# Optimization experiments

Hardware: AMD Instinct MI355X
Metric: run time of the kernel (lower is better)

Reference implementation:

```python
import jax, jax.numpy as jnp
import numpy as np

N_NODES = 40000
N_EDGES = 640000
BATCH = 2
IN_DIM = 3
HID = 128
OUT_DIM = 3


def setup_inputs() -> dict:
    key = jax.random.key(0)
    ks = jax.random.split(key, 16)
    p = jax.random.normal(ks[0], (BATCH, N_NODES, IN_DIM), dtype=jnp.float32)
    edge_rows = jax.random.randint(ks[1], (N_EDGES,), 0, N_NODES, dtype=jnp.int32)
    edge_cols = jax.random.randint(ks[2], (N_EDGES,), 0, N_NODES, dtype=jnp.int32)
    # normalize_sparse_matrix: divide each nonzero (value 1.0) by the row's nonzero count
    deg = jax.ops.segment_sum(jnp.ones((N_EDGES,), jnp.float32), edge_rows, num_segments=N_NODES)
    adj_vals = 1.0 / deg[edge_rows]  # every used row has deg >= 1
    s = 0.05
    # initial Linear(3 -> 128)
    W_init = jax.random.normal(ks[3], (IN_DIM, HID), jnp.float32) * s
    b_init = jnp.zeros((HID,), jnp.float32)
    # 4 GraphConvs inside the two blocks (all 128->128), each has filter + self_filter
    Wf_blocks = jax.random.normal(ks[4], (4, HID, HID), jnp.float32) * s
    bf_blocks = jnp.zeros((4, HID), jnp.float32)
    Ws_blocks = jax.random.normal(ks[5], (4, HID, HID), jnp.float32) * s
    bs_blocks = jnp.zeros((4, HID), jnp.float32)
    # final GraphConvLayer (128 -> 3)
    Wf_out = jax.random.normal(ks[6], (HID, OUT_DIM), jnp.float32) * s
    bf_out = jnp.zeros((OUT_DIM,), jnp.float32)
    Ws_out = jax.random.normal(ks[7], (HID, OUT_DIM), jnp.float32) * s
    bs_out = jnp.zeros((OUT_DIM,), jnp.float32)
    return dict(p=p, adj_vals=adj_vals, edge_rows=edge_rows, edge_cols=edge_cols,
                W_init=W_init, b_init=b_init,
                Wf_blocks=Wf_blocks, bf_blocks=bf_blocks,
                Ws_blocks=Ws_blocks, bs_blocks=bs_blocks,
                Wf_out=Wf_out, bf_out=bf_out, Ws_out=Ws_out, bs_out=bs_out)


def reference(p, adj_vals, edge_rows, edge_cols,
              W_init, b_init,
              Wf_blocks, bf_blocks, Ws_blocks, bs_blocks,
              Wf_out, bf_out, Ws_out, bs_out):
    n = p.shape[1]

    def spmm(xb):  # xb: [N, d] -> A @ xb via edge-list scatter-add
        return jax.ops.segment_sum(adj_vals[:, None] * xb[edge_cols], edge_rows, num_segments=n)

    spmm_b = jax.vmap(spmm)  # [B, N, d]

    def gconv(x, Wf, bf, Ws, bs):
        # sparse path: self_filter(x) + filter(spmm(adj, x))
        return (x @ Ws + bs) + (spmm_b(x) @ Wf + bf)

    x = p @ W_init + b_init  # [B, N, HID]
    for blk in range(2):  # two GraphConvBlocks, residual, no shortcut (dims equal)
        net = gconv(jax.nn.relu(x), Wf_blocks[2 * blk], bf_blocks[2 * blk],
                    Ws_blocks[2 * blk], bs_blocks[2 * blk])
        dx = gconv(jax.nn.relu(net), Wf_blocks[2 * blk + 1], bf_blocks[2 * blk + 1],
                   Ws_blocks[2 * blk + 1], bs_blocks[2 * blk + 1])
        x = x + dx
    # final GraphConvLayer 128 -> 3
    out = gconv(jax.nn.relu(x), Wf_out, bf_out, Ws_out, bs_out)
    return out
```

## Files before the change

### kernel.cpp

```cpp
#include <hip/hip_runtime.h>


typedef unsigned short u16;
typedef unsigned int   u32;
typedef __bf16 bf8_t __attribute__((ext_vector_type(8)));
typedef float  f4_t  __attribute__((ext_vector_type(4)));

#define N_NODES 40000
#define N_EDGES 640000
#define BN      80000

__device__ __forceinline__ float bf2f(u16 u) {
  union { u32 i; float f; } v; v.i = ((u32)u) << 16; return v.f;
}
__device__ __forceinline__ u16 f2bf(float f) {
  union { float f; u32 i; } v; v.f = f;
  u32 i = v.i;
  return (u16)((i + 0x7FFFu + ((i >> 16) & 1u)) >> 16);
}
__device__ __forceinline__ float asf(u32 i) {
  union { u32 u; float f; } v; v.u = i; return v.f;
}
__device__ __forceinline__ u32 pack2(float a, float b) {
  return (u32)f2bf(a) | ((u32)f2bf(b) << 16);
}

__global__ void fill_kernel(float* __restrict__ out, int n, float v) {
  int i = blockIdx.x * 256 + threadIdx.x;
  if (i < n) out[i] = v;
}

__global__ void hist_kernel(const int* __restrict__ rows, int* __restrict__ cnt) {
  int e = blockIdx.x * 256 + threadIdx.x;
  if (e < N_EDGES) atomicAdd(&cnt[rows[e]], 1);
}

__global__ void scan1_kernel(const int* __restrict__ cnt, int* __restrict__ row_ptr,
                             int* __restrict__ blocksum) {
  __shared__ int sm[256];
  int t = threadIdx.x;
  int row = blockIdx.x * 256 + t;
  int v = (row < N_NODES) ? cnt[row] : 0;
  sm[t] = v; __syncthreads();
  for (int off = 1; off < 256; off <<= 1) {
    int u = (t >= off) ? sm[t - off] : 0;
    __syncthreads();
    sm[t] += u;
    __syncthreads();
  }
  if (row < N_NODES) row_ptr[row] = sm[t] - v;
  if (t == 255) blocksum[blockIdx.x] = sm[255];
}

__global__ void scan2_kernel(int* __restrict__ blocksum, int* __restrict__ row_ptr, int nblk) {
  __shared__ int sm[256];
  int t = threadIdx.x;
  int v = (t < nblk) ? blocksum[t] : 0;
  sm[t] = v; __syncthreads();
  for (int off = 1; off < 256; off <<= 1) {
    int u = (t >= off) ? sm[t - off] : 0;
    __syncthreads();
    sm[t] += u;
    __syncthreads();
  }
  if (t < nblk) blocksum[t] = sm[t] - v;
  if (t == 255) row_ptr[N_NODES] = sm[255];
}

__global__ void scan3_kernel(int* __restrict__ row_ptr, const int* __restrict__ blocksum,
                             int* __restrict__ cnt) {
  int row = blockIdx.x * 256 + threadIdx.x;
  if (row < N_NODES) {
    int rp = row_ptr[row] + blocksum[blockIdx.x];
    row_ptr[row] = rp;
    cnt[row] = rp;
  }
}

__global__ void scatter_kernel(const int* __restrict__ rows, const int* __restrict__ cols,
                               int* __restrict__ cur, int* __restrict__ cols_s) {
  int e = blockIdx.x * 256 + threadIdx.x;
  if (e < N_EDGES) {
    int r = rows[e];
    int pos = atomicAdd(&cur[r], 1);
    cols_s[pos] = cols[e];
  }
}

__global__ void wprep_kernel(const float* __restrict__ Wf_b, const float* __restrict__ Ws_b,
                             const float* __restrict__ bf_b, const float* __restrict__ bs_b,
                             u16* __restrict__ WtCat, float* __restrict__ biasCat) {
  int idx = blockIdx.x * 256 + threadIdx.x;
  int g = idx >> 15, rem = idx & 32767;
  int h = rem >> 8, k = rem & 255;
  float v = (k < 128) ? Ws_b[(g * 128 + k) * 128 + h]
                      : Wf_b[(g * 128 + (k - 128)) * 128 + h];
  WtCat[idx] = f2bf(v);
  if (k == 0) biasCat[g * 128 + h] = bs_b[g * 128 + h] + bf_b[g * 128 + h];
}

__global__ void init_kernel(const float* __restrict__ p, const float* __restrict__ W,
                            const float* __restrict__ bias, u16* __restrict__ xb,
                            u16* __restrict__ rA) {
  int idx = blockIdx.x * 256 + threadIdx.x;
  int row = idx >> 6;
  int h = (idx & 63) * 2;
  float p0 = p[row * 3], p1 = p[row * 3 + 1], p2 = p[row * 3 + 2];
  float s0 = p0 * W[h]     + p1 * W[128 + h]     + p2 * W[256 + h]     + bias[h];
  float s1 = p0 * W[h + 1] + p1 * W[128 + h + 1] + p2 * W[256 + h + 1] + bias[h + 1];
  size_t o = (size_t)row * 64 + (h >> 1);
  ((u32*)xb)[o] = pack2(s0, s1);
  ((u32*)rA)[o] = pack2(s0 > 0.f ? s0 : 0.f, s1 > 0.f ? s1 : 0.f);
}

__global__ void spmm_kernel(const int* __restrict__ row_ptr, const int* __restrict__ cols_s,
                            const u16* __restrict__ xin, u16* __restrict__ yout) {
  int row = blockIdx.x * 4 + (threadIdx.x >> 6);
  int l = threadIdx.x & 63;
  int b = l >> 5, seg = l & 31;
  int s = row_ptr[row], e = row_ptr[row + 1];
  const u32* X = (const u32*)xin + (size_t)b * 2560000 + seg * 2;
  float a0 = 0.f, a1 = 0.f, a2 = 0.f, a3 = 0.f;
  int i = s;
  for (; i + 1 < e; i += 2) {
    int c0 = cols_s[i], c1 = cols_s[i + 1];
    uint2 u0 = *reinterpret_cast<const uint2*>(X + (size_t)c0 * 64);
    uint2 u1 = *reinterpret_cast<const uint2*>(X + (size_t)c1 * 64);
    a0 += asf(u0.x << 16); a1 += asf(u0.x & 0xffff0000u);
    a2 += asf(u0.y << 16); a3 += asf(u0.y & 0xffff0000u);
    a0 += asf(u1.x << 16); a1 += asf(u1.x & 0xffff0000u);
    a2 += asf(u1.y << 16); a3 += asf(u1.y & 0xffff0000u);
  }
  if (i < e) {
    int c = cols_s[i];
    uint2 u = *reinterpret_cast<const uint2*>(X + (size_t)c * 64);
    a0 += asf(u.x << 16); a1 += asf(u.x & 0xffff0000u);
    a2 += asf(u.y << 16); a3 += asf(u.y & 0xffff0000u);
  }
  float scale = (e > s) ? 1.f / (float)(e - s) : 0.f;
  uint2 o;
  o.x = pack2(a0 * scale, a1 * scale);
  o.y = pack2(a2 * scale, a3 * scale);
  *reinterpret_cast<uint2*>((u32*)yout + (size_t)b * 2560000 + (size_t)row * 64 + seg * 2) = o;
}

template <int MODE>
__global__ __launch_bounds__(256, 2) void gemm_kernel(
    const u16* __restrict__ rin, const u16* __restrict__ yin,
    const u16* __restrict__ WtCat, const float* __restrict__ biasCat, int g,
    u16* __restrict__ rout, u16* __restrict__ xresid) {
  __shared__ __align__(16) u16 ldsA[128 * 72];
  __shared__ __align__(16) u16 ldsW[128 * 72];
  int tid = threadIdx.x;
  int m0 = blockIdx.x * 128;
  int li = tid & 15, q = (tid >> 4) & 3, wv = tid >> 6;
  int wmo = (wv >> 1) * 64, wno = (wv & 1) * 64;

  f4_t acc[4][4];
#pragma unroll
  for (int i = 0; i < 4; ++i)
#pragma unroll
    for (int j = 0; j < 4; ++j) acc[i][j] = (f4_t){0.f, 0.f, 0.f, 0.f};

  const u16* Wsrc = WtCat + (size_t)g * 32768;

  for (int kb = 0; kb < 256; kb += 64) {
    __syncthreads();
    const u16* srcA = (kb < 128) ? (rin + kb) : (yin + (kb - 128));
#pragma unroll
    for (int p2 = 0; p2 < 4; ++p2) {
      int idx = p2 * 256 + tid;
      int row = idx >> 3, seg = idx & 7;
      uint4 va = *reinterpret_cast<const uint4*>(srcA + (size_t)(m0 + row) * 128 + seg * 8);
      *reinterpret_cast<uint4*>(&ldsA[row * 72 + seg * 8]) = va;
      uint4 vw = *reinterpret_cast<const uint4*>(Wsrc + (size_t)row * 256 + kb + seg * 8);
      *reinterpret_cast<uint4*>(&ldsW[row * 72 + seg * 8]) = vw;
    }
    __syncthreads();
#pragma unroll
    for (int kk = 0; kk < 64; kk += 32) {
      bf8_t af[4], wf[4];
#pragma unroll
      for (int t = 0; t < 4; ++t)
        af[t] = __builtin_bit_cast(bf8_t,
            *reinterpret_cast<const uint4*>(&ldsA[(wmo + t * 16 + li) * 72 + kk + q * 8]));
#pragma unroll
      for (int t = 0; t < 4; ++t)
        wf[t] = __builtin_bit_cast(bf8_t,
            *reinterpret_cast<const uint4*>(&ldsW[(wno + t * 16 + li) * 72 + kk + q * 8]));
#pragma unroll
      for (int i = 0; i < 4; ++i)
#pragma unroll
        for (int j = 0; j < 4; ++j)
          acc[i][j] = __builtin_amdgcn_mfma_f32_16x16x32_bf16(af[i], wf[j], acc[i][j], 0, 0, 0);
    }
  }

  float bias[4];
#pragma unroll
  for (int j = 0; j < 4; ++j) bias[j] = biasCat[g * 128 + wno + j * 16 + li];

#pragma unroll
  for (int i = 0; i < 4; ++i)
#pragma unroll
    for (int j = 0; j < 4; ++j)
#pragma unroll
      for (int r2 = 0; r2 < 4; ++r2) {
        int m = m0 + wmo + i * 16 + q * 4 + r2;
        int col = wno + j * 16 + li;
        float c = acc[i][j][r2] + bias[j];
        size_t id = (size_t)m * 128 + col;
        if (MODE == 0) {
          rout[id] = f2bf(c > 0.f ? c : 0.f);
        } else {
          float xn = bf2f(xresid[id]) + c;
          xresid[id] = f2bf(xn);
          rout[id] = f2bf(xn > 0.f ? xn : 0.f);
        }
      }
}

__global__ void final_kernel(const u16* __restrict__ rA, const u16* __restrict__ y,
                             const float* __restrict__ Wso, const float* __restrict__ Wfo,
                             const float* __restrict__ bso, const float* __restrict__ bfo,
                             float* __restrict__ out) {
  int row = blockIdx.x * 4 + (threadIdx.x >> 6);
  int l = threadIdx.x & 63;
  u32 ra = ((const u32*)rA)[(size_t)row * 64 + l];
  u32 yv = ((const u32*)y)[(size_t)row * 64 + l];
  float r0 = asf(ra << 16), r1 = asf(ra & 0xffff0000u);
  float y0 = asf(yv << 16), y1 = asf(yv & 0xffff0000u);
  int ch = l * 2;
  float p0 = r0 * Wso[ch * 3 + 0] + y0 * Wfo[ch * 3 + 0] + r1 * Wso[ch * 3 + 3] + y1 * Wfo[ch * 3 + 3];
  float p1 = r0 * Wso[ch * 3 + 1] + y0 * Wfo[ch * 3 + 1] + r1 * Wso[ch * 3 + 4] + y1 * Wfo[ch * 3 + 4];
  float p2 = r0 * Wso[ch * 3 + 2] + y0 * Wfo[ch * 3 + 2] + r1 * Wso[ch * 3 + 5] + y1 * Wfo[ch * 3 + 5];
#pragma unroll
  for (int off = 32; off >= 1; off >>= 1) {
    p0 += __shfl_down(p0, off);
    p1 += __shfl_down(p1, off);
    p2 += __shfl_down(p2, off);
  }
  if (l == 0) {
    out[row * 3 + 0] = p0 + bso[0] + bfo[0];
    out[row * 3 + 1] = p1 + bso[1] + bfo[1];
    out[row * 3 + 2] = p2 + bso[2] + bfo[2];
  }
}

extern "C" void kernel_launch(void* const* d_in, const int* in_sizes, int n_in,
                              void* d_out, int out_size, void* d_ws, size_t ws_size,
                              hipStream_t stream) {
  float* out = (float*)d_out;
  int fill_grid = (out_size + 255) / 256;

  const int exp_sizes[14] = {240000, 640000, 640000, 640000, 384, 128,
                             65536, 512, 65536, 512, 384, 3, 384, 3};
  bool sizes_ok = (n_in == 14);
  if (sizes_ok) for (int i = 0; i < 14; ++i) if (in_sizes[i] != exp_sizes[i]) sizes_ok = false;
  if (!sizes_ok) {
    fill_kernel<<<fill_grid, 256, 0, stream>>>(out, out_size, 1.0f);
    return;
  }

  const size_t NEED = (size_t)4 * BN * 128 * 2 + (size_t)N_EDGES * 4 + 160016 + 160000 + 1024 + 262144 + 2048;
  if (ws_size < NEED) {
    fill_kernel<<<fill_grid, 256, 0, stream>>>(out, out_size, 0.0f);
    return;
  }

  const float* p      = (const float*)d_in[0];
  const int*   erows  = (const int*)d_in[2];
  const int*   ecols  = (const int*)d_in[3];
  const float* W_init = (const float*)d_in[4];
  const float* b_init = (const float*)d_in[5];
  const float* Wf_b   = (const float*)d_in[6];
  const float* bf_b   = (const float*)d_in[7];
  const float* Ws_b   = (const float*)d_in[8];
  const float* bs_b   = (const float*)d_in[9];
  const float* Wf_o   = (const float*)d_in[10];
  const float* bf_o   = (const float*)d_in[11];
  const float* Ws_o   = (const float*)d_in[12];
  const float* bs_o   = (const float*)d_in[13];

  char* w = (char*)d_ws;
  u16*   rA       = (u16*)w;   w += (size_t)BN * 128 * 2;
  u16*   rB       = (u16*)w;   w += (size_t)BN * 128 * 2;
  u16*   y        = (u16*)w;   w += (size_t)BN * 128 * 2;
  u16*   xb       = (u16*)w;   w += (size_t)BN * 128 * 2;
  int*   cols_s   = (int*)w;   w += (size_t)N_EDGES * 4;
  int*   row_ptr  = (int*)w;   w += 160016;
  int*   cnt      = (int*)w;   w += 160000;
  int*   blocksum = (int*)w;   w += 1024;
  u16*   WtCat    = (u16*)w;   w += 4 * 128 * 256 * 2;
  float* biasCat  = (float*)w; w += 4 * 128 * 4;

  const int NBLK = (N_NODES + 255) / 256;

  hipMemsetAsync(cnt, 0, N_NODES * 4, stream);
  hist_kernel<<<2500, 256, 0, stream>>>(erows, cnt);
  scan1_kernel<<<NBLK, 256, 0, stream>>>(cnt, row_ptr, blocksum);
  scan2_kernel<<<1, 256, 0, stream>>>(blocksum, row_ptr, NBLK);
  scan3_kernel<<<NBLK, 256, 0, stream>>>(row_ptr, blocksum, cnt);
  scatter_kernel<<<2500, 256, 0, stream>>>(erows, ecols, cnt, cols_s);
  wprep_kernel<<<512, 256, 0, stream>>>(Wf_b, Ws_b, bf_b, bs_b, WtCat, biasCat);
  init_kernel<<<20000, 256, 0, stream>>>(p, W_init, b_init, xb, rA);

  for (int blk = 0; blk < 2; ++blk) {
    spmm_kernel<<<10000, 256, 0, stream>>>(row_ptr, cols_s, rA, y);
    gemm_kernel<0><<<625, 256, 0, stream>>>(rA, y, WtCat, biasCat, 2 * blk, rB, nullptr);
    spmm_kernel<<<10000, 256, 0, stream>>>(row_ptr, cols_s, rB, y);
    gemm_kernel<1><<<625, 256, 0, stream>>>(rB, y, WtCat, biasCat, 2 * blk + 1, rA, xb);
  }
  spmm_kernel<<<10000, 256, 0, stream>>>(row_ptr, cols_s, rA, y);
  final_kernel<<<20000, 256, 0, stream>>>(rA, y, Ws_o, Wf_o, bs_o, bf_o, out);
}
```

Measured before the change: 510.0 us.

## Sort edges by column bucket, split SpMM per batch, project before final SpMM

CSR construction now buckets each row's edges into 8 column ranges, so neighbor gathers within a row are roughly ordered by column, which should help cache locality. The SpMM kernel gives each batch its own block, with one u32 per lane and the loop unrolled by four. The final layer projects to 3 channels before aggregating, because A(xW) = (Ax)W, so the last SpMM gathers 16-byte float4 rows instead of 256-byte rows. The costs are an 8x larger count array, extra scan kernels in setup, and a different fp32 summation order in the last layer.

Result: no change. 510.1 us (+0.0%).

```diff
diff --git a/kernel.cpp b/kernel.cpp
--- a/kernel.cpp
+++ b/kernel.cpp
@@ -9,6 +9,7 @@
 #define N_NODES 40000
 #define N_EDGES 640000
 #define BN      80000
+#define SCAN_N  320000
 
 __device__ __forceinline__ float bf2f(u16 u) {
   union { u32 i; float f; } v; v.i = ((u32)u) << 16; return v.f;
@@ -30,29 +31,31 @@
   if (i < n) out[i] = v;
 }
 
-__global__ void hist_kernel(const int* __restrict__ rows, int* __restrict__ cnt) {
+__global__ void hist2_kernel(const int* __restrict__ rows, const int* __restrict__ cols,
+                             int* __restrict__ cnt2) {
   int e = blockIdx.x * 256 + threadIdx.x;
-  if (e < N_EDGES) atomicAdd(&cnt[rows[e]], 1);
-}
-
-__global__ void scan1_kernel(const int* __restrict__ cnt, int* __restrict__ row_ptr,
-                             int* __restrict__ blocksum) {
+  if (e < N_EDGES) {
+    int t = cols[e] >> 13;
+    atomicAdd(&cnt2[rows[e] * 8 + t], 1);
+  }
+}
+
+__global__ void scanA_kernel(const int* __restrict__ cnt2, int* __restrict__ blocksum) {
   __shared__ int sm[256];
   int t = threadIdx.x;
-  int row = blockIdx.x * 256 + t;
-  int v = (row < N_NODES) ? cnt[row] : 0;
-  sm[t] = v; __syncthreads();
-  for (int off = 1; off < 256; off <<= 1) {
-    int u = (t >= off) ? sm[t - off] : 0;
-    __syncthreads();
-    sm[t] += u;
-    __syncthreads();
-  }
-  if (row < N_NODES) row_ptr[row] = sm[t] - v;
-  if (t == 255) blocksum[blockIdx.x] = sm[255];
-}
-
-__global__ void scan2_kernel(int* __restrict__ blocksum, int* __restrict__ row_ptr, int nblk) {
+  int base = blockIdx.x * 2048 + t * 8;
+  int s = 0;
+#pragma unroll
+  for (int i = 0; i < 8; ++i) { int idx = base + i; if (idx < SCAN_N) s += cnt2[idx]; }
+  sm[t] = s; __syncthreads();
+  for (int off = 128; off > 0; off >>= 1) {
+    if (t < off) sm[t] += sm[t + off];
+    __syncthreads();
+  }
+  if (t == 0) blocksum[blockIdx.x] = sm[0];
+}
+
+__global__ void scanB_kernel(int* __restrict__ blocksum, int nblk) {
   __shared__ int sm[256];
   int t = threadIdx.x;
   int v = (t < nblk) ? blocksum[t] : 0;
@@ -64,26 +67,44 @@
     __syncthreads();
   }
   if (t < nblk) blocksum[t] = sm[t] - v;
-  if (t == 255) row_ptr[N_NODES] = sm[255];
-}
-
-__global__ void scan3_kernel(int* __restrict__ row_ptr, const int* __restrict__ blocksum,
-                             int* __restrict__ cnt) {
-  int row = blockIdx.x * 256 + threadIdx.x;
-  if (row < N_NODES) {
-    int rp = row_ptr[row] + blocksum[blockIdx.x];
-    row_ptr[row] = rp;
-    cnt[row] = rp;
-  }
-}
-
-__global__ void scatter_kernel(const int* __restrict__ rows, const int* __restrict__ cols,
-                               int* __restrict__ cur, int* __restrict__ cols_s) {
+}
+
+__global__ void scanC_kernel(int* __restrict__ cnt2, const int* __restrict__ blocksum) {
+  __shared__ int sm[256];
+  int t = threadIdx.x;
+  int base = blockIdx.x * 2048 + t * 8;
+  int v[8]; int s = 0;
+#pragma unroll
+  for (int i = 0; i < 8; ++i) { int idx = base + i; v[i] = (idx < SCAN_N) ? cnt2[idx] : 0; s += v[i]; }
+  sm[t] = s; __syncthreads();
+  for (int off = 1; off < 256; off <<= 1) {
+    int u = (t >= off) ? sm[t - off] : 0;
+    __syncthreads();
+    sm[t] += u;
+    __syncthreads();
+  }
+  int run = blocksum[blockIdx.x] + sm[t] - s;
+#pragma unroll
+  for (int i = 0; i < 8; ++i) {
+    int idx = base + i;
+    if (idx < SCAN_N) { int c = v[i]; cnt2[idx] = run; run += c; }
+  }
+}
+
+__global__ void rowptr_kernel(const int* __restrict__ cnt2, int* __restrict__ row_ptr) {
+  int r = blockIdx.x * 256 + threadIdx.x;
+  if (r < N_NODES) row_ptr[r] = cnt2[r * 8];
+  if (r == 0) row_ptr[N_NODES] = N_EDGES;
+}
+
+__global__ void scatter2_kernel(const int* __restrict__ rows, const int* __restrict__ cols,
+                                int* __restrict__ cur2, int* __restrict__ cols_s) {
   int e = blockIdx.x * 256 + threadIdx.x;
   if (e < N_EDGES) {
-    int r = rows[e];
-    int pos = atomicAdd(&cur[r], 1);
-    cols_s[pos] = cols[e];
+    int c = cols[e];
+    int t = c >> 13;
+    int pos = atomicAdd(&cur2[rows[e] * 8 + t], 1);
+    cols_s[pos] = c;
   }
 }
 
@@ -115,33 +136,27 @@
 
 __global__ void spmm_kernel(const int* __restrict__ row_ptr, const int* __restrict__ cols_s,
                             const u16* __restrict__ xin, u16* __restrict__ yout) {
-  int row = blockIdx.x * 4 + (threadIdx.x >> 6);
+  int b = blockIdx.x & 1;
+  int row = (blockIdx.x >> 1) * 4 + (threadIdx.x >> 6);
   int l = threadIdx.x & 63;
-  int b = l >> 5, seg = l & 31;
   int s = row_ptr[row], e = row_ptr[row + 1];
-  const u32* X = (const u32*)xin + (size_t)b * 2560000 + seg * 2;
-  float a0 = 0.f, a1 = 0.f, a2 = 0.f, a3 = 0.f;
+  const u32* X = (const u32*)xin + (size_t)b * 2560000 + l;
+  float a0 = 0.f, a1 = 0.f;
   int i = s;
-  for (; i + 1 < e; i += 2) {
-    int c0 = cols_s[i], c1 = cols_s[i + 1];
-    uint2 u0 = *reinterpret_cast<const uint2*>(X + (size_t)c0 * 64);
-    uint2 u1 = *reinterpret_cast<const uint2*>(X + (size_t)c1 * 64);
-    a0 += asf(u0.x << 16); a1 += asf(u0.x & 0xffff0000u);
-    a2 += asf(u0.y << 16); a3 += asf(u0.y & 0xffff0000u);
-    a0 += asf(u1.x << 16); a1 += asf(u1.x & 0xffff0000u);
-    a2 += asf(u1.y << 16); a3 += asf(u1.y & 0xffff0000u);
-  }
-  if (i < e) {
-    int c = cols_s[i];
-    uint2 u = *reinterpret_cast<const uint2*>(X + (size_t)c * 64);
-    a0 += asf(u.x << 16); a1 += asf(u.x & 0xffff0000u);
-    a2 += asf(u.y << 16); a3 += asf(u.y & 0xffff0000u);
+  for (; i + 3 < e; i += 4) {
+    int c0 = cols_s[i], c1 = cols_s[i + 1], c2 = cols_s[i + 2], c3 = cols_s[i + 3];
+    u32 u0 = X[c0 * 64], u1 = X[c1 * 64], u2 = X[c2 * 64], u3 = X[c3 * 64];
+    a0 += asf(u0 << 16); a1 += asf(u0 & 0xffff0000u);
+    a0 += asf(u1 << 16); a1 += asf(u1 & 0xffff0000u);
+    a0 += asf(u2 << 16); a1 += asf(u2 & 0xffff0000u);
+    a0 += asf(u3 << 16); a1 += asf(u3 & 0xffff0000u);
+  }
+  for (; i < e; ++i) {
+    u32 u = X[cols_s[i] * 64];
+    a0 += asf(u << 16); a1 += asf(u & 0xffff0000u);
   }
   float scale = (e > s) ? 1.f / (float)(e - s) : 0.f;
-  uint2 o;
-  o.x = pack2(a0 * scale, a1 * scale);
-  o.y = pack2(a2 * scale, a3 * scale);
-  *reinterpret_cast<uint2*>((u32*)yout + (size_t)b * 2560000 + (size_t)row * 64 + seg * 2) = o;
+  ((u32*)yout)[(size_t)b * 2560000 + (size_t)row * 64 + l] = pack2(a0 * scale, a1 * scale);
 }
 
 template <int MODE>
@@ -220,31 +235,51 @@
       }
 }
 
-__global__ void final_kernel(const u16* __restrict__ rA, const u16* __restrict__ y,
-                             const float* __restrict__ Wso, const float* __restrict__ Wfo,
-                             const float* __restrict__ bso, const float* __restrict__ bfo,
-                             float* __restrict__ out) {
+__global__ void zproj_kernel(const u16* __restrict__ rA,
+                             const float* __restrict__ Wfo, const float* __restrict__ Wso,
+                             const float* __restrict__ bfo, const float* __restrict__ bso,
+                             float4* __restrict__ zf4, float4* __restrict__ zs4) {
   int row = blockIdx.x * 4 + (threadIdx.x >> 6);
   int l = threadIdx.x & 63;
   u32 ra = ((const u32*)rA)[(size_t)row * 64 + l];
-  u32 yv = ((const u32*)y)[(size_t)row * 64 + l];
   float r0 = asf(ra << 16), r1 = asf(ra & 0xffff0000u);
-  float y0 = asf(yv << 16), y1 = asf(yv & 0xffff0000u);
   int ch = l * 2;
-  float p0 = r0 * Wso[ch * 3 + 0] + y0 * Wfo[ch * 3 + 0] + r1 * Wso[ch * 3 + 3] + y1 * Wfo[ch * 3 + 3];
-  float p1 = r0 * Wso[ch * 3 + 1] + y0 * Wfo[ch * 3 + 1] + r1 * Wso[ch * 3 + 4] + y1 * Wfo[ch * 3 + 4];
-  float p2 = r0 * Wso[ch * 3 + 2] + y0 * Wfo[ch * 3 + 2] + r1 * Wso[ch * 3 + 5] + y1 * Wfo[ch * 3 + 5];
+  float f0 = r0 * Wfo[ch * 3 + 0] + r1 * Wfo[ch * 3 + 3];
+  float f1 = r0 * Wfo[ch * 3 + 1] + r1 * Wfo[ch * 3 + 4];
+  float f2 = r0 * Wfo[ch * 3 + 2] + r1 * Wfo[ch * 3 + 5];
+  float s0 = r0 * Wso[ch * 3 + 0] + r1 * Wso[ch * 3 + 3];
+  float s1 = r0 * Wso[ch * 3 + 1] + r1 * Wso[ch * 3 + 4];
+  float s2 = r0 * Wso[ch * 3 + 2] + r1 * Wso[ch * 3 + 5];
 #pragma unroll
   for (int off = 32; off >= 1; off >>= 1) {
-    p0 += __shfl_down(p0, off);
-    p1 += __shfl_down(p1, off);
-    p2 += __shfl_down(p2, off);
+    f0 += __shfl_down(f0, off); f1 += __shfl_down(f1, off); f2 += __shfl_down(f2, off);
+    s0 += __shfl_down(s0, off); s1 += __shfl_down(s1, off); s2 += __shfl_down(s2, off);
   }
   if (l == 0) {
-    out[row * 3 + 0] = p0 + bso[0] + bfo[0];
-    out[row * 3 + 1] = p1 + bso[1] + bfo[1];
-    out[row * 3 + 2] = p2 + bso[2] + bfo[2];
-  }
+    zf4[row] = make_float4(f0, f1, f2, 0.f);
+    zs4[row] = make_float4(s0 + bso[0] + bfo[0], s1 + bso[1] + bfo[1], s2 + bso[2] + bfo[2], 0.f);
+  }
+}
+
+__global__ void spmm3_kernel(const int* __restrict__ row_ptr, const int* __restrict__ cols_s,
+                             const float4* __restrict__ zf4, const float4* __restrict__ zs4,
+                             float* __restrict__ out) {
+  int idx = blockIdx.x * 256 + threadIdx.x;
+  if (idx >= BN) return;
+  int b = (idx >= N_NODES) ? 1 : 0;
+  int r = idx - b * N_NODES;
+  int s = row_ptr[r], e = row_ptr[r + 1];
+  const float4* Z = zf4 + (size_t)b * N_NODES;
+  float a0 = 0.f, a1 = 0.f, a2 = 0.f;
+  for (int i = s; i < e; ++i) {
+    float4 z = Z[cols_s[i]];
+    a0 += z.x; a1 += z.y; a2 += z.z;
+  }
+  float sc = (e > s) ? 1.f / (float)(e - s) : 0.f;
+  float4 zs = zs4[idx];
+  out[idx * 3 + 0] = zs.x + a0 * sc;
+  out[idx * 3 + 1] = zs.y + a1 * sc;
+  out[idx * 3 + 2] = zs.z + a2 * sc;
 }
 
 extern "C" void kernel_launch(void* const* d_in, const int* in_sizes, int n_in,
@@ -262,7 +297,8 @@
     return;
   }
 
-  const size_t NEED = (size_t)4 * BN * 128 * 2 + (size_t)N_EDGES * 4 + 160016 + 160000 + 1024 + 262144 + 2048;
+  const size_t NEED = (size_t)4 * BN * 128 * 2 + (size_t)N_EDGES * 4 + 160016
+                    + (size_t)N_NODES * 8 * 4 + 1024 + 262144 + 2048;
   if (ws_size < NEED) {
     fill_kernel<<<fill_grid, 256, 0, stream>>>(out, out_size, 0.0f);
     return;
@@ -289,28 +325,32 @@
   u16*   xb       = (u16*)w;   w += (size_t)BN * 128 * 2;
   int*   cols_s   = (int*)w;   w += (size_t)N_EDGES * 4;
   int*   row_ptr  = (int*)w;   w += 160016;
-  int*   cnt      = (int*)w;   w += 160000;
+  int*   cnt2     = (int*)w;   w += (size_t)N_NODES * 8 * 4;
   int*   blocksum = (int*)w;   w += 1024;
   u16*   WtCat    = (u16*)w;   w += 4 * 128 * 256 * 2;
   float* biasCat  = (float*)w; w += 4 * 128 * 4;
 
-  const int NBLK = (N_NODES + 255) / 256;
-
-  hipMemsetAsync(cnt, 0, N_NODES * 4, stream);
-  hist_kernel<<<2500, 256, 0, stream>>>(erows, cnt);
-  scan1_kernel<<<NBLK, 256, 0, stream>>>(cnt, row_ptr, blocksum);
-  scan2_kernel<<<1, 256, 0, stream>>>(blocksum, row_ptr, NBLK);
-  scan3_kernel<<<NBLK, 256, 0, stream>>>(row_ptr, blocksum, cnt);
-  scatter_kernel<<<2500, 256, 0, stream>>>(erows, ecols, cnt, cols_s);
+  float4* zf4 = (float4*)y;
+  float4* zs4 = (float4*)(y + 640000);
+
+  const int SBLK = (SCAN_N + 2047) / 2048;
+
+  hipMemsetAsync(cnt2, 0, (size_t)N_NODES * 8 * 4, stream);
+  hist2_kernel<<<2500, 256, 0, stream>>>(erows, ecols, cnt2);
+  scanA_kernel<<<SBLK, 256, 0, stream>>>(cnt2, blocksum);
+  scanB_kernel<<<1, 256, 0, stream>>>(blocksum, SBLK);
+  scanC_kernel<<<SBLK, 256, 0, stream>>>(cnt2, blocksum);
+  rowptr_kernel<<<157, 256, 0, stream>>>(cnt2, row_ptr);
+  scatter2_kernel<<<2500, 256, 0, stream>>>(erows, ecols, cnt2, cols_s);
   wprep_kernel<<<512, 256, 0, stream>>>(Wf_b, Ws_b, bf_b, bs_b, WtCat, biasCat);
   init_kernel<<<20000, 256, 0, stream>>>(p, W_init, b_init, xb, rA);
 
   for (int blk = 0; blk < 2; ++blk) {
-    spmm_kernel<<<10000, 256, 0, stream>>>(row_ptr, cols_s, rA, y);
+    spmm_kernel<<<20000, 256, 0, stream>>>(row_ptr, cols_s, rA, y);
     gemm_kernel<0><<<625, 256, 0, stream>>>(rA, y, WtCat, biasCat, 2 * blk, rB, nullptr);
-    spmm_kernel<<<10000, 256, 0, stream>>>(row_ptr, cols_s, rB, y);
+    spmm_kernel<<<20000, 256, 0, stream>>>(row_ptr, cols_s, rB, y);
     gemm_kernel<1><<<625, 256, 0, stream>>>(rB, y, WtCat, biasCat, 2 * blk + 1, rA, xb);
   }
-  spmm_kernel<<<10000, 256, 0, stream>>>(row_ptr, cols_s, rA, y);
-  final_kernel<<<20000, 256, 0, stream>>>(rA, y, Ws_o, Wf_o, bs_o, bf_o, out);
-}
+  zproj_kernel<<<20000, 256, 0, stream>>>(rA, Wf_o, Ws_o, bf_o, bs_o, zf4, zs4);
+  spmm3_kernel<<<(BN + 255) / 256, 256, 0, stream>>>(row_ptr, cols_s, zf4, zs4, out);
+}
```
